# Performance work log

Measured on AMD Instinct MI355X. Metric: run time of the kernel, lower is better.

Reference implementation:

```python
import jax, jax.numpy as jnp
import numpy as np

N_GRAPHS = 64


def gcn_conv(x, W, b, src, dst, n_nodes):
    """PyG GCNConv: add self-loops, symmetric D^-1/2 (A+I) D^-1/2 normalization,
    linear transform, scatter-add aggregation at target nodes, plus bias."""
    xw = x @ W  # [N, out]  transform before propagate (PyG order)
    loop = jnp.arange(n_nodes, dtype=src.dtype)
    rows = jnp.concatenate([src, loop])  # message sources
    cols = jnp.concatenate([dst, loop])  # message targets
    deg = jax.ops.segment_sum(jnp.ones_like(cols, dtype=xw.dtype), cols,
                              num_segments=n_nodes)
    dinv = jnp.where(deg > 0, jax.lax.rsqrt(deg), 0.0)
    norm = dinv[rows] * dinv[cols]  # [E+N]
    msgs = norm[:, None] * xw[rows]  # gather + scale
    out = jax.ops.segment_sum(msgs, cols, num_segments=n_nodes)  # scatter-add
    return out + b


def global_mean_pool(x, batch, n_graphs):
    sums = jax.ops.segment_sum(x, batch, num_segments=n_graphs)
    cnts = jax.ops.segment_sum(jnp.ones((x.shape[0],), x.dtype), batch,
                               num_segments=n_graphs)
    return sums / jnp.maximum(cnts, 1.0)[:, None]


def setup_inputs() -> dict:
    key = jax.random.key(0)
    k1, k2, k3, k4, k5, k6 = jax.random.split(key, 6)
    N, E = 50000, 800000
    d_in, d_hid, d_out = 128, 128, 64
    x = jax.random.normal(k1, (N, d_in), dtype=jnp.float32)
    edge_index = jax.random.randint(k2, (2, E), 0, N, dtype=jnp.int64)
    batch = jnp.sort(jax.random.randint(k3, (N,), 0, N_GRAPHS, dtype=jnp.int64))
    # Glorot-ish init for GCN weights, zero bias (PyG default)
    W1 = jax.random.normal(k4, (d_in, d_hid), dtype=jnp.float32) / np.sqrt(d_in)
    b1 = jnp.zeros((d_hid,), jnp.float32)
    W2 = jax.random.normal(k5, (d_hid, d_out), dtype=jnp.float32) / np.sqrt(d_hid)
    b2 = jnp.zeros((d_out,), jnp.float32)
    return {"x": x, "edge_index": edge_index, "batch": batch,
            "W1": W1, "b1": b1, "W2": W2, "b2": b2}


def reference(x, edge_index, batch, W1, b1, W2, b2):
    n_nodes = x.shape[0]
    src, dst = edge_index[0], edge_index[1]
    h = jax.nn.relu(gcn_conv(x, W1, b1, src, dst, n_nodes))
    h = gcn_conv(h, W2, b2, src, dst, n_nodes)
    return global_mean_pool(h, batch, N_GRAPHS)
```

## Files before the change

### kernel.cpp

```cpp
#include <hip/hip_runtime.h>
#include <hip/hip_fp16.h>

typedef __attribute__((ext_vector_type(8))) short bf16x8;
typedef __attribute__((ext_vector_type(4))) float f32x4;

__device__ __forceinline__ unsigned short f2bf(float f) {
  unsigned u = __float_as_uint(f);
  u += 0x7FFFu + ((u >> 16) & 1u);
  return (unsigned short)(u >> 16);
}
__device__ __forceinline__ float bflo(unsigned u) { return __uint_as_float(u << 16); }
__device__ __forceinline__ float bfhi(unsigned u) { return __uint_as_float(u & 0xFFFF0000u); }
__device__ __forceinline__ float unpackw(unsigned pk) {
  return __half2float(__ushort_as_half((unsigned short)(pk >> 16)));
}

template <int CO, bool AF32>
__device__ __forceinline__ void gemm_body(const void* __restrict__ Aptr,
                                          const float* __restrict__ W,
                                          unsigned short* __restrict__ Y, int N,
                                          int bid, int tid, unsigned short* Wl) {
  constexpr int K = 128;
  constexpr int SP = K + 8;
  for (int i = tid; i < K * CO; i += 256) {
    int k = i / CO, n = i % CO;
    Wl[n * SP + k] = f2bf(W[i]);
  }
  __syncthreads();

  const int lane = tid & 63;
  const int quad = lane >> 4, l16 = lane & 15;
  const int mbase = bid * 64 + (tid >> 6) * 16;
  const int arow = min(mbase + l16, N - 1);

  bf16x8 afrag[4];
  if constexpr (AF32) {
    const float* A = (const float*)Aptr + (size_t)arow * K;
#pragma unroll
    for (int ks = 0; ks < 4; ks++) {
      const float4* p = (const float4*)(A + ks * 32 + quad * 8);
      float4 f0 = p[0], f1 = p[1];
      afrag[ks] = (bf16x8){(short)f2bf(f0.x), (short)f2bf(f0.y), (short)f2bf(f0.z), (short)f2bf(f0.w),
                           (short)f2bf(f1.x), (short)f2bf(f1.y), (short)f2bf(f1.z), (short)f2bf(f1.w)};
    }
  } else {
    const unsigned short* A = (const unsigned short*)Aptr + (size_t)arow * K;
#pragma unroll
    for (int ks = 0; ks < 4; ks++) afrag[ks] = *(const bf16x8*)(A + ks * 32 + quad * 8);
  }

#pragma unroll
  for (int ct = 0; ct < CO / 16; ct++) {
    f32x4 acc = {0.0f, 0.0f, 0.0f, 0.0f};
#pragma unroll
    for (int ks = 0; ks < 4; ks++) {
      bf16x8 b = *(const bf16x8*)(&Wl[(ct * 16 + l16) * SP + ks * 32 + quad * 8]);
      acc = __builtin_amdgcn_mfma_f32_16x16x32_bf16(afrag[ks], b, acc, 0, 0, 0);
    }
#pragma unroll
    for (int reg = 0; reg < 4; reg++) {
      int node = mbase + quad * 4 + reg;
      if (node < N) Y[(size_t)node * CO + ct * 16 + l16] = f2bf(acc[reg]);
    }
  }
}

__global__ __launch_bounds__(256) void k_mega1(const float* __restrict__ x,
                                               const float* __restrict__ W1,
                                               unsigned short* __restrict__ xw1b, int N,
                                               const int* __restrict__ src,
                                               const int* __restrict__ dst,
                                               int* __restrict__ cnt,
                                               unsigned short* __restrict__ colsrc, int E,
                                               const int* __restrict__ batch,
                                               int* __restrict__ firstIdx,
                                               int gM, int gE4) {
  __shared__ unsigned short Wl[128 * 136];
  const int bid = blockIdx.x, tid = threadIdx.x;
  if (bid < gM) {
    gemm_body<128, true>(x, W1, xw1b, N, bid, tid, Wl);
  } else if (bid < gM + gE4) {
    int e0 = (bid - gM) * 1024 + tid * 4;
    if (e0 + 3 < E) {
      int4 d4 = *(const int4*)(dst + e0);
      int4 s4 = *(const int4*)(src + e0);
      int r;
      r = atomicAdd(&cnt[d4.x], 1); if (r < 64) colsrc[(d4.x << 6) + r] = (unsigned short)s4.x;
      r = atomicAdd(&cnt[d4.y], 1); if (r < 64) colsrc[(d4.y << 6) + r] = (unsigned short)s4.y;
      r = atomicAdd(&cnt[d4.z], 1); if (r < 64) colsrc[(d4.z << 6) + r] = (unsigned short)s4.z;
      r = atomicAdd(&cnt[d4.w], 1); if (r < 64) colsrc[(d4.w << 6) + r] = (unsigned short)s4.w;
    } else {
      for (int e = e0; e < E; e++) {
        int d = dst[e];
        int r = atomicAdd(&cnt[d], 1);
        if (r < 64) colsrc[(d << 6) + r] = (unsigned short)src[e];
      }
    }
  } else {
    int n = (bid - gM - gE4) * 256 + tid;
    if (n < N) {
      int b = batch[n];
      if (n == 0 || batch[n - 1] != b) firstIdx[b] = n + 1;
    }
  }
}

__global__ __launch_bounds__(256) void k_agg128(const unsigned short* __restrict__ xwb,
                                                const int* __restrict__ cnt,
                                                const unsigned short* __restrict__ colsrc,
                                                const float* __restrict__ bias,
                                                unsigned short* __restrict__ out, int N) {
  const int tid = threadIdx.x;
  const int lane = tid & 63;
  const int gl = lane & 15;
  const int grp = lane >> 4;
  const int wv = tid >> 6;
  const int v = blockIdx.x * 16 + wv * 4 + grp;
  const int vc = min(v, N - 1);

  const int c = cnt[vc];
  const int jc = (v < N) ? min(c, 64) : 0;
  const float dv = rsqrtf((float)(c + 1));

  float acc[8];
  {
    const float d2 = dv * dv;
    uint4 s = *(const uint4*)((const char*)xwb + (((size_t)vc << 8) | (gl << 4)));
    acc[0] = d2 * bflo(s.x); acc[1] = d2 * bfhi(s.x);
    acc[2] = d2 * bflo(s.y); acc[3] = d2 * bfhi(s.y);
    acc[4] = d2 * bflo(s.z); acc[5] = d2 * bfhi(s.z);
    acc[6] = d2 * bflo(s.w); acc[7] = d2 * bfhi(s.w);
  }

  const int gbase = grp << 4;
  for (int base = 0; __any(base < jc); base += 16) {
    unsigned pk0 = 0u;
    if (base + gl < jc) {
      int s = colsrc[(vc << 6) + base + gl];
      float ws = rsqrtf((float)(cnt[s] + 1)) * dv;
      pk0 = (unsigned)s | ((unsigned)__half_as_ushort(__float2half_rn(ws)) << 16);
    }
    int mv = jc - base;
    mv = mv < 0 ? 0 : (mv > 16 ? 16 : mv);
    int mm = max(mv, __shfl_xor(mv, 16, 64));
    mm = max(mm, __shfl_xor(mm, 32, 64));
    const int rp = (mm + 7) & ~7;
    for (int t = 0; t < rp; t += 8) {
      uint4 rbuf[8];
      float wbuf[8];
#pragma unroll
      for (int r = 0; r < 8; r++) {
        unsigned pk = (unsigned)__shfl((int)pk0, gbase + t + r, 64);
        wbuf[r] = unpackw(pk);
        rbuf[r] = *(const uint4*)((const char*)xwb + (((pk & 0xFFFFu) << 8) | (gl << 4)));
      }
#pragma unroll
      for (int r = 0; r < 8; r++) {
        const float w = wbuf[r];
        const uint4 rr = rbuf[r];
        acc[0] += w * bflo(rr.x); acc[1] += w * bfhi(rr.x);
        acc[2] += w * bflo(rr.y); acc[3] += w * bfhi(rr.y);
        acc[4] += w * bflo(rr.z); acc[5] += w * bfhi(rr.z);
        acc[6] += w * bflo(rr.w); acc[7] += w * bfhi(rr.w);
      }
    }
  }

  if (v < N) {
    float4 b0 = ((const float4*)bias)[gl * 2];
    float4 b1 = ((const float4*)bias)[gl * 2 + 1];
    float a0 = fmaxf(acc[0] + b0.x, 0.f), a1 = fmaxf(acc[1] + b0.y, 0.f);
    float a2 = fmaxf(acc[2] + b0.z, 0.f), a3 = fmaxf(acc[3] + b0.w, 0.f);
    float a4 = fmaxf(acc[4] + b1.x, 0.f), a5 = fmaxf(acc[5] + b1.y, 0.f);
    float a6 = fmaxf(acc[6] + b1.z, 0.f), a7 = fmaxf(acc[7] + b1.w, 0.f);
    uint4 st;
    st.x = (unsigned)f2bf(a0) | ((unsigned)f2bf(a1) << 16);
    st.y = (unsigned)f2bf(a2) | ((unsigned)f2bf(a3) << 16);
    st.z = (unsigned)f2bf(a4) | ((unsigned)f2bf(a5) << 16);
    st.w = (unsigned)f2bf(a6) | ((unsigned)f2bf(a7) << 16);
    *(uint4*)((char*)out + (((size_t)v << 8) | (gl << 4))) = st;
  }
}

__global__ __launch_bounds__(256) void k_aggpool2(const unsigned short* __restrict__ h1b,
                                                  const int* __restrict__ cnt,
                                                  const unsigned short* __restrict__ colsrc,
                                                  const int* __restrict__ batch,
                                                  float* __restrict__ stage, int N) {
  __shared__ float sAcc[4][128];
  const int tid = threadIdx.x;
  const int lane = tid & 63;
  const int gl = lane & 15;
  const int grp = lane >> 4;
  const int wv = tid >> 6;
  const int v = blockIdx.x * 16 + wv * 4 + grp;
  const int vc = min(v, N - 1);

  const int c = cnt[vc];
  const int jc = (v < N) ? min(c, 64) : 0;
  const float dv = rsqrtf((float)(c + 1));

  float acc[8];
  {
    const float d2 = (v < N) ? dv * dv : 0.0f;
    uint4 s = *(const uint4*)((const char*)h1b + (((size_t)vc << 8) | (gl << 4)));
    acc[0] = d2 * bflo(s.x); acc[1] = d2 * bfhi(s.x);
    acc[2] = d2 * bflo(s.y); acc[3] = d2 * bfhi(s.y);
    acc[4] = d2 * bflo(s.z); acc[5] = d2 * bfhi(s.z);
    acc[6] = d2 * bflo(s.w); acc[7] = d2 * bfhi(s.w);
  }

  const int gbase = grp << 4;
  for (int base = 0; __any(base < jc); base += 16) {
    unsigned pk0 = 0u;
    if (base + gl < jc) {
      int s = colsrc[(vc << 6) + base + gl];
      float ws = rsqrtf((float)(cnt[s] + 1)) * dv;
      pk0 = (unsigned)s | ((unsigned)__half_as_ushort(__float2half_rn(ws)) << 16);
    }
    int mv = jc - base;
    mv = mv < 0 ? 0 : (mv > 16 ? 16 : mv);
    int mm = max(mv, __shfl_xor(mv, 16, 64));
    mm = max(mm, __shfl_xor(mm, 32, 64));
    const int rp = (mm + 7) & ~7;
    for (int t = 0; t < rp; t += 8) {
      uint4 rbuf[8];
      float wbuf[8];
#pragma unroll
      for (int r = 0; r < 8; r++) {
        unsigned pk = (unsigned)__shfl((int)pk0, gbase + t + r, 64);
        wbuf[r] = unpackw(pk);
        rbuf[r] = *(const uint4*)((const char*)h1b + (((pk & 0xFFFFu) << 8) | (gl << 4)));
      }
#pragma unroll
      for (int r = 0; r < 8; r++) {
        const float w = wbuf[r];
        const uint4 rr = rbuf[r];
        acc[0] += w * bflo(rr.x); acc[1] += w * bfhi(rr.x);
        acc[2] += w * bflo(rr.y); acc[3] += w * bfhi(rr.y);
        acc[4] += w * bflo(rr.z); acc[5] += w * bfhi(rr.z);
        acc[6] += w * bflo(rr.w); acc[7] += w * bfhi(rr.w);
      }
    }
  }

  const int v0 = blockIdx.x * 16;
  const bool uniform = (v0 + 15 < N) && (batch[v0] == batch[v0 + 15]);
  if (uniform) {
#pragma unroll
    for (int d = 16; d < 64; d <<= 1)
#pragma unroll
      for (int k = 0; k < 8; k++) acc[k] += __shfl_xor(acc[k], d, 64);
    if (grp == 0) {
#pragma unroll
      for (int k = 0; k < 8; k++) sAcc[wv][gl * 8 + k] = acc[k];
    }
    __syncthreads();
    if (wv == 0) {
      const int g = batch[v0];
      float t0 = sAcc[0][lane] + sAcc[1][lane] + sAcc[2][lane] + sAcc[3][lane];
      float t1 = sAcc[0][lane + 64] + sAcc[1][lane + 64] + sAcc[2][lane + 64] + sAcc[3][lane + 64];
      atomicAdd(&stage[g * 128 + lane], t0);
      atomicAdd(&stage[g * 128 + lane + 64], t1);
    }
  } else if (v < N) {
    const int b = batch[vc];
#pragma unroll
    for (int k = 0; k < 8; k++) atomicAdd(&stage[b * 128 + gl * 8 + k], acc[k]);
  }
}

__global__ void k_wout(const float* __restrict__ stage, const int* __restrict__ firstIdx,
                       const float* __restrict__ W2, const float* __restrict__ b2,
                       float* __restrict__ out, int N) {
  __shared__ float denom[64];
  __shared__ float red[256];
  const int tid = threadIdx.x;
  const int g = blockIdx.x;
  if (tid < 64) {
    int raw = firstIdx[tid];
    int fi = (raw > 0) ? raw - 1 : 0x7FFFFFFF;
    int m = fi;
#pragma unroll
    for (int d = 1; d < 64; d <<= 1) {
      int t = __shfl_down(m, d, 64);
      if (tid + d < 64) m = min(m, t);
    }
    int nxtm = __shfl_down(m, 1, 64);
    int nxt = (tid == 63) ? N : min(nxtm, N);
    int c = (fi == 0x7FFFFFFF) ? 0 : (nxt - fi);
    denom[tid] = fmaxf((float)c, 1.0f);
  }
  __syncthreads();
  const int j = tid & 63, kc = tid >> 6;
  float p = 0.0f;
#pragma unroll 8
  for (int k = kc * 32; k < kc * 32 + 32; k++)
    p += stage[g * 128 + k] * W2[k * 64 + j];
  red[tid] = p;
  __syncthreads();
  if (tid < 64) {
    float t = red[tid] + red[tid + 64] + red[tid + 128] + red[tid + 192];
    out[g * 64 + tid] = t / denom[g] + b2[tid];
  }
}


extern "C" void kernel_launch(void* const* d_in, const int* in_sizes, int n_in,
                              void* d_out, int out_size, void* d_ws, size_t ws_size,
                              hipStream_t stream) {
  const float* x     = (const float*)d_in[0];
  const int*   ei    = (const int*)d_in[1];
  const int*   batch = (const int*)d_in[2];
  const float* W1    = (const float*)d_in[3];
  const float* b1    = (const float*)d_in[4];
  const float* W2    = (const float*)d_in[5];
  const float* b2    = (const float*)d_in[6];

  const int N = in_sizes[2];
  const int E = in_sizes[1] / 2;
  const int* src  = ei;
  const int* dstv = ei + E;

  unsigned short* xw1b = (unsigned short*)d_ws;
  unsigned short* h1b  = xw1b + (size_t)N * 128;
  int*   cnt     = (int*)(h1b + (size_t)N * 128);
  int*   firstIdx= cnt + N;
  float* stage   = (float*)(firstIdx + 64);
  unsigned short* colsrc = (unsigned short*)(stage + 64 * 128);
  float* outp    = (float*)d_out;

  hipMemsetAsync(cnt, 0, (size_t)(N + 64 + 64 * 128) * sizeof(int), stream);

  const int gM  = (N + 63) / 64;
  const int gE4 = (E + 1023) / 1024;
  const int gN  = (N + 255) / 256;
  const int gA1 = (N + 15) / 16;

  k_mega1<<<gM + gE4 + gN, 256, 0, stream>>>(x, W1, xw1b, N, src, dstv, cnt,
                                             colsrc, E, batch, firstIdx, gM, gE4);

  k_agg128<<<gA1, 256, 0, stream>>>(xw1b, cnt, colsrc, b1, h1b, N);

  k_aggpool2<<<gA1, 256, 0, stream>>>(h1b, cnt, colsrc, batch, stage, N);

  k_wout<<<64, 256, 0, stream>>>(stage, firstIdx, W2, b2, outp, N);
}
```

Baseline: 190.2 us.

## Prefetch neighbor list once and double-buffer gather loads in aggregation kernels

Each lane now loads four neighbor indices at once with a ushort4 read and computes all their packed weights up front, replacing the per-16-neighbor chunk loop. The gather loop is double-buffered: the next batch of eight neighbor rows is loaded while FMAs run on the current batch, to hide gather latency. The cost is more live registers (two uint4[8] buffers), which may reduce occupancy.

```diff
diff --git a/kernel.cpp b/kernel.cpp
--- a/kernel.cpp
+++ b/kernel.cpp
@@ -105,6 +105,68 @@
   }
 }
 
+#define AGG_PREP(XWB_SHIFT)                                                         \
+  ushort4 s4v = *(const ushort4*)(colsrc + ((size_t)vc << 6) + gl * 4);             \
+  unsigned pk4[4];                                                                  \
+  {                                                                                 \
+    unsigned short se[4] = {s4v.x, s4v.y, s4v.z, s4v.w};                            \
+_Pragma("unroll")                                                                   \
+    for (int k = 0; k < 4; k++) {                                                   \
+      unsigned pk = 0u;                                                             \
+      int e = gl * 4 + k;                                                           \
+      if (e < jc) {                                                                 \
+        int s = se[k];                                                              \
+        float ws = rsqrtf((float)(cnt[s] + 1)) * dv;                                \
+        pk = (unsigned)s | ((unsigned)__half_as_ushort(__float2half_rn(ws)) << 16); \
+      }                                                                             \
+      pk4[k] = pk;                                                                  \
+    }                                                                               \
+  }                                                                                 \
+  int mm = jc;                                                                      \
+  mm = max(mm, __shfl_xor(mm, 16, 64));                                             \
+  mm = max(mm, __shfl_xor(mm, 32, 64));                                             \
+  const int nb = (mm + 7) >> 3;
+
+#define AGG_LOADB(bexp, R, WB, BASE, XWB_SHIFT)                                     \
+  {                                                                                 \
+    const int bb_ = (bexp);                                                         \
+_Pragma("unroll")                                                                   \
+    for (int r = 0; r < 8; r++) {                                                   \
+      unsigned pk = (unsigned)__shfl((int)pk4[r & 3], gbase + 2 * bb_ + (r >> 2), 64); \
+      WB[r] = unpackw(pk);                                                          \
+      R[r] = *(const uint4*)((const char*)(BASE) + (((pk & 0xFFFFu) << (XWB_SHIFT)) | (gl << 4))); \
+    }                                                                               \
+  }
+
+#define AGG_FMA(R, WB)                                                              \
+_Pragma("unroll")                                                                   \
+  for (int r = 0; r < 8; r++) {                                                     \
+    const float w = WB[r];                                                          \
+    const uint4 rr = R[r];                                                          \
+    acc[0] += w * bflo(rr.x); acc[1] += w * bfhi(rr.x);                             \
+    acc[2] += w * bflo(rr.y); acc[3] += w * bfhi(rr.y);                             \
+    acc[4] += w * bflo(rr.z); acc[5] += w * bfhi(rr.z);                             \
+    acc[6] += w * bflo(rr.w); acc[7] += w * bfhi(rr.w);                             \
+  }
+
+#define AGG_PIPELINE(BASE, XWB_SHIFT)                                               \
+  uint4 rA[8], rB[8];                                                               \
+  float wA[8], wB[8];                                                               \
+  if (nb > 0) {                                                                     \
+    AGG_LOADB(0, rA, wA, BASE, XWB_SHIFT);                                          \
+    int b = 0;                                                                      \
+    while (true) {                                                                  \
+      if (b + 1 < nb) AGG_LOADB(b + 1, rB, wB, BASE, XWB_SHIFT);                    \
+      AGG_FMA(rA, wA);                                                              \
+      b++;                                                                          \
+      if (b >= nb) break;                                                           \
+      if (b + 1 < nb) AGG_LOADB(b + 1, rA, wA, BASE, XWB_SHIFT);                    \
+      AGG_FMA(rB, wB);                                                              \
+      b++;                                                                          \
+      if (b >= nb) break;                                                           \
+    }                                                                               \
+  }
+
 __global__ __launch_bounds__(256) void k_agg128(const unsigned short* __restrict__ xwb,
                                                 const int* __restrict__ cnt,
                                                 const unsigned short* __restrict__ colsrc,
@@ -121,6 +183,7 @@
   const int c = cnt[vc];
   const int jc = (v < N) ? min(c, 64) : 0;
   const float dv = rsqrtf((float)(c + 1));
+  const int gbase = grp << 4;
 
   float acc[8];
   {
@@ -132,39 +195,8 @@
     acc[6] = d2 * bflo(s.w); acc[7] = d2 * bfhi(s.w);
   }
 
-  const int gbase = grp << 4;
-  for (int base = 0; __any(base < jc); base += 16) {
-    unsigned pk0 = 0u;
-    if (base + gl < jc) {
-      int s = colsrc[(vc << 6) + base + gl];
-      float ws = rsqrtf((float)(cnt[s] + 1)) * dv;
-      pk0 = (unsigned)s | ((unsigned)__half_as_ushort(__float2half_rn(ws)) << 16);
-    }
-    int mv = jc - base;
-    mv = mv < 0 ? 0 : (mv > 16 ? 16 : mv);
-    int mm = max(mv, __shfl_xor(mv, 16, 64));
-    mm = max(mm, __shfl_xor(mm, 32, 64));
-    const int rp = (mm + 7) & ~7;
-    for (int t = 0; t < rp; t += 8) {
-      uint4 rbuf[8];
-      float wbuf[8];
-#pragma unroll
-      for (int r = 0; r < 8; r++) {
-        unsigned pk = (unsigned)__shfl((int)pk0, gbase + t + r, 64);
-        wbuf[r] = unpackw(pk);
-        rbuf[r] = *(const uint4*)((const char*)xwb + (((pk & 0xFFFFu) << 8) | (gl << 4)));
-      }
-#pragma unroll
-      for (int r = 0; r < 8; r++) {
-        const float w = wbuf[r];
-        const uint4 rr = rbuf[r];
-        acc[0] += w * bflo(rr.x); acc[1] += w * bfhi(rr.x);
-        acc[2] += w * bflo(rr.y); acc[3] += w * bfhi(rr.y);
-        acc[4] += w * bflo(rr.z); acc[5] += w * bfhi(rr.z);
-        acc[6] += w * bflo(rr.w); acc[7] += w * bfhi(rr.w);
-      }
-    }
-  }
+  AGG_PREP(8)
+  AGG_PIPELINE(xwb, 8)
 
   if (v < N) {
     float4 b0 = ((const float4*)bias)[gl * 2];
@@ -199,6 +231,7 @@
   const int c = cnt[vc];
   const int jc = (v < N) ? min(c, 64) : 0;
   const float dv = rsqrtf((float)(c + 1));
+  const int gbase = grp << 4;
 
   float acc[8];
   {
@@ -210,39 +243,8 @@
     acc[6] = d2 * bflo(s.w); acc[7] = d2 * bfhi(s.w);
   }
 
-  const int gbase = grp << 4;
-  for (int base = 0; __any(base < jc); base += 16) {
-    unsigned pk0 = 0u;
-    if (base + gl < jc) {
-      int s = colsrc[(vc << 6) + base + gl];
-      float ws = rsqrtf((float)(cnt[s] + 1)) * dv;
-      pk0 = (unsigned)s | ((unsigned)__half_as_ushort(__float2half_rn(ws)) << 16);
-    }
-    int mv = jc - base;
-    mv = mv < 0 ? 0 : (mv > 16 ? 16 : mv);
-    int mm = max(mv, __shfl_xor(mv, 16, 64));
-    mm = max(mm, __shfl_xor(mm, 32, 64));
-    const int rp = (mm + 7) & ~7;
-    for (int t = 0; t < rp; t += 8) {
-      uint4 rbuf[8];
-      float wbuf[8];
-#pragma unroll
-      for (int r = 0; r < 8; r++) {
-        unsigned pk = (unsigned)__shfl((int)pk0, gbase + t + r, 64);
-        wbuf[r] = unpackw(pk);
-        rbuf[r] = *(const uint4*)((const char*)h1b + (((pk & 0xFFFFu) << 8) | (gl << 4)));
-      }
-#pragma unroll
-      for (int r = 0; r < 8; r++) {
-        const float w = wbuf[r];
-        const uint4 rr = rbuf[r];
-        acc[0] += w * bflo(rr.x); acc[1] += w * bfhi(rr.x);
-        acc[2] += w * bflo(rr.y); acc[3] += w * bfhi(rr.y);
-        acc[4] += w * bflo(rr.z); acc[5] += w * bfhi(rr.z);
-        acc[6] += w * bflo(rr.w); acc[7] += w * bfhi(rr.w);
-      }
-    }
-  }
+  AGG_PREP(8)
+  AGG_PIPELINE(h1b, 8)
 
   const int v0 = blockIdx.x * 16;
   const bool uniform = (v0 + 15 < N) && (batch[v0] == batch[v0 + 15]);
```

After: 202.1 us. 1.06x slower.

## Replace second-layer gather and pool with a graph-coefficient matrix and pooled GEMM

Applied to the files above, without the earlier changes.

The second GCN aggregation followed by mean pooling is rewritten algebraically. A per-node coefficient matrix Ct[N,64] is built by atomically adding each edge's normalisation weight (and the self-loop weight) into the column of the target node's graph. The pooled features then become Ct^T·h1, computed by a streaming partial-GEMM kernel with 256 blocks and reduced in k_wout. The Ct build is folded into the layer-1 aggregation launch, so the random 128-wide neighbour gathers of layer two are removed. In exchange it adds a 12.8 MB memset, 800k scattered float atomics, a larger workspace, and a GEMM with limited block parallelism.

```diff
diff --git a/kernel.cpp b/kernel.cpp
--- a/kernel.cpp
+++ b/kernel.cpp
@@ -11,6 +11,7 @@
 }
 __device__ __forceinline__ float bflo(unsigned u) { return __uint_as_float(u << 16); }
 __device__ __forceinline__ float bfhi(unsigned u) { return __uint_as_float(u & 0xFFFF0000u); }
+__device__ __forceinline__ float bf1(unsigned short h) { return __uint_as_float(((unsigned)h) << 16); }
 __device__ __forceinline__ float unpackw(unsigned pk) {
   return __half2float(__ushort_as_half((unsigned short)(pk >> 16)));
 }
@@ -105,175 +106,163 @@
   }
 }
 
-__global__ __launch_bounds__(256) void k_agg128(const unsigned short* __restrict__ xwb,
-                                                const int* __restrict__ cnt,
-                                                const unsigned short* __restrict__ colsrc,
-                                                const float* __restrict__ bias,
-                                                unsigned short* __restrict__ out, int N) {
-  const int tid = threadIdx.x;
-  const int lane = tid & 63;
-  const int gl = lane & 15;
-  const int grp = lane >> 4;
-  const int wv = tid >> 6;
-  const int v = blockIdx.x * 16 + wv * 4 + grp;
-  const int vc = min(v, N - 1);
-
-  const int c = cnt[vc];
-  const int jc = (v < N) ? min(c, 64) : 0;
-  const float dv = rsqrtf((float)(c + 1));
-
-  float acc[8];
-  {
-    const float d2 = dv * dv;
-    uint4 s = *(const uint4*)((const char*)xwb + (((size_t)vc << 8) | (gl << 4)));
-    acc[0] = d2 * bflo(s.x); acc[1] = d2 * bfhi(s.x);
-    acc[2] = d2 * bflo(s.y); acc[3] = d2 * bfhi(s.y);
-    acc[4] = d2 * bflo(s.z); acc[5] = d2 * bfhi(s.z);
-    acc[6] = d2 * bflo(s.w); acc[7] = d2 * bfhi(s.w);
-  }
-
-  const int gbase = grp << 4;
-  for (int base = 0; __any(base < jc); base += 16) {
-    unsigned pk0 = 0u;
-    if (base + gl < jc) {
-      int s = colsrc[(vc << 6) + base + gl];
-      float ws = rsqrtf((float)(cnt[s] + 1)) * dv;
-      pk0 = (unsigned)s | ((unsigned)__half_as_ushort(__float2half_rn(ws)) << 16);
-    }
-    int mv = jc - base;
-    mv = mv < 0 ? 0 : (mv > 16 ? 16 : mv);
-    int mm = max(mv, __shfl_xor(mv, 16, 64));
-    mm = max(mm, __shfl_xor(mm, 32, 64));
-    const int rp = (mm + 7) & ~7;
-    for (int t = 0; t < rp; t += 8) {
-      uint4 rbuf[8];
-      float wbuf[8];
-#pragma unroll
-      for (int r = 0; r < 8; r++) {
-        unsigned pk = (unsigned)__shfl((int)pk0, gbase + t + r, 64);
-        wbuf[r] = unpackw(pk);
-        rbuf[r] = *(const uint4*)((const char*)xwb + (((pk & 0xFFFFu) << 8) | (gl << 4)));
-      }
-#pragma unroll
-      for (int r = 0; r < 8; r++) {
-        const float w = wbuf[r];
-        const uint4 rr = rbuf[r];
-        acc[0] += w * bflo(rr.x); acc[1] += w * bfhi(rr.x);
-        acc[2] += w * bflo(rr.y); acc[3] += w * bfhi(rr.y);
-        acc[4] += w * bflo(rr.z); acc[5] += w * bfhi(rr.z);
-        acc[6] += w * bflo(rr.w); acc[7] += w * bfhi(rr.w);
-      }
-    }
-  }
-
-  if (v < N) {
-    float4 b0 = ((const float4*)bias)[gl * 2];
-    float4 b1 = ((const float4*)bias)[gl * 2 + 1];
-    float a0 = fmaxf(acc[0] + b0.x, 0.f), a1 = fmaxf(acc[1] + b0.y, 0.f);
-    float a2 = fmaxf(acc[2] + b0.z, 0.f), a3 = fmaxf(acc[3] + b0.w, 0.f);
-    float a4 = fmaxf(acc[4] + b1.x, 0.f), a5 = fmaxf(acc[5] + b1.y, 0.f);
-    float a6 = fmaxf(acc[6] + b1.z, 0.f), a7 = fmaxf(acc[7] + b1.w, 0.f);
-    uint4 st;
-    st.x = (unsigned)f2bf(a0) | ((unsigned)f2bf(a1) << 16);
-    st.y = (unsigned)f2bf(a2) | ((unsigned)f2bf(a3) << 16);
-    st.z = (unsigned)f2bf(a4) | ((unsigned)f2bf(a5) << 16);
-    st.w = (unsigned)f2bf(a6) | ((unsigned)f2bf(a7) << 16);
-    *(uint4*)((char*)out + (((size_t)v << 8) | (gl << 4))) = st;
-  }
-}
-
-__global__ __launch_bounds__(256) void k_aggpool2(const unsigned short* __restrict__ h1b,
-                                                  const int* __restrict__ cnt,
-                                                  const unsigned short* __restrict__ colsrc,
-                                                  const int* __restrict__ batch,
-                                                  float* __restrict__ stage, int N) {
-  __shared__ float sAcc[4][128];
-  const int tid = threadIdx.x;
-  const int lane = tid & 63;
-  const int gl = lane & 15;
-  const int grp = lane >> 4;
-  const int wv = tid >> 6;
-  const int v = blockIdx.x * 16 + wv * 4 + grp;
-  const int vc = min(v, N - 1);
-
-  const int c = cnt[vc];
-  const int jc = (v < N) ? min(c, 64) : 0;
-  const float dv = rsqrtf((float)(c + 1));
-
-  float acc[8];
-  {
-    const float d2 = (v < N) ? dv * dv : 0.0f;
-    uint4 s = *(const uint4*)((const char*)h1b + (((size_t)vc << 8) | (gl << 4)));
-    acc[0] = d2 * bflo(s.x); acc[1] = d2 * bfhi(s.x);
-    acc[2] = d2 * bflo(s.y); acc[3] = d2 * bfhi(s.y);
-    acc[4] = d2 * bflo(s.z); acc[5] = d2 * bfhi(s.z);
-    acc[6] = d2 * bflo(s.w); acc[7] = d2 * bfhi(s.w);
-  }
-
-  const int gbase = grp << 4;
-  for (int base = 0; __any(base < jc); base += 16) {
-    unsigned pk0 = 0u;
-    if (base + gl < jc) {
-      int s = colsrc[(vc << 6) + base + gl];
-      float ws = rsqrtf((float)(cnt[s] + 1)) * dv;
-      pk0 = (unsigned)s | ((unsigned)__half_as_ushort(__float2half_rn(ws)) << 16);
-    }
-    int mv = jc - base;
-    mv = mv < 0 ? 0 : (mv > 16 ? 16 : mv);
-    int mm = max(mv, __shfl_xor(mv, 16, 64));
-    mm = max(mm, __shfl_xor(mm, 32, 64));
-    const int rp = (mm + 7) & ~7;
-    for (int t = 0; t < rp; t += 8) {
-      uint4 rbuf[8];
-      float wbuf[8];
-#pragma unroll
-      for (int r = 0; r < 8; r++) {
-        unsigned pk = (unsigned)__shfl((int)pk0, gbase + t + r, 64);
-        wbuf[r] = unpackw(pk);
-        rbuf[r] = *(const uint4*)((const char*)h1b + (((pk & 0xFFFFu) << 8) | (gl << 4)));
-      }
-#pragma unroll
-      for (int r = 0; r < 8; r++) {
-        const float w = wbuf[r];
-        const uint4 rr = rbuf[r];
-        acc[0] += w * bflo(rr.x); acc[1] += w * bfhi(rr.x);
-        acc[2] += w * bflo(rr.y); acc[3] += w * bfhi(rr.y);
-        acc[4] += w * bflo(rr.z); acc[5] += w * bfhi(rr.z);
-        acc[6] += w * bflo(rr.w); acc[7] += w * bfhi(rr.w);
-      }
-    }
-  }
-
-  const int v0 = blockIdx.x * 16;
-  const bool uniform = (v0 + 15 < N) && (batch[v0] == batch[v0 + 15]);
-  if (uniform) {
-#pragma unroll
-    for (int d = 16; d < 64; d <<= 1)
-#pragma unroll
-      for (int k = 0; k < 8; k++) acc[k] += __shfl_xor(acc[k], d, 64);
-    if (grp == 0) {
-#pragma unroll
-      for (int k = 0; k < 8; k++) sAcc[wv][gl * 8 + k] = acc[k];
-    }
-    __syncthreads();
-    if (wv == 0) {
-      const int g = batch[v0];
-      float t0 = sAcc[0][lane] + sAcc[1][lane] + sAcc[2][lane] + sAcc[3][lane];
-      float t1 = sAcc[0][lane + 64] + sAcc[1][lane + 64] + sAcc[2][lane + 64] + sAcc[3][lane + 64];
-      atomicAdd(&stage[g * 128 + lane], t0);
-      atomicAdd(&stage[g * 128 + lane + 64], t1);
-    }
-  } else if (v < N) {
-    const int b = batch[vc];
-#pragma unroll
-    for (int k = 0; k < 8; k++) atomicAdd(&stage[b * 128 + gl * 8 + k], acc[k]);
-  }
-}
-
-__global__ void k_wout(const float* __restrict__ stage, const int* __restrict__ firstIdx,
+__global__ __launch_bounds__(256) void k_mega2(const unsigned short* __restrict__ xwb,
+                                               const int* __restrict__ cnt,
+                                               const unsigned short* __restrict__ colsrc,
+                                               const float* __restrict__ bias,
+                                               unsigned short* __restrict__ out, int N,
+                                               const int* __restrict__ src,
+                                               const int* __restrict__ dst,
+                                               const int* __restrict__ batch,
+                                               float* __restrict__ Ct, int E,
+                                               int gA, int gE4) {
+  const int bid = blockIdx.x, tid = threadIdx.x;
+  if (bid < gA) {
+    const int lane = tid & 63;
+    const int gl = lane & 15;
+    const int grp = lane >> 4;
+    const int wv = tid >> 6;
+    const int v = bid * 16 + wv * 4 + grp;
+    const int vc = min(v, N - 1);
+
+    const int c = cnt[vc];
+    const int jc = (v < N) ? min(c, 64) : 0;
+    const float dv = rsqrtf((float)(c + 1));
+
+    float acc[8];
+    {
+      const float d2 = dv * dv;
+      uint4 s = *(const uint4*)((const char*)xwb + (((size_t)vc << 8) | (gl << 4)));
+      acc[0] = d2 * bflo(s.x); acc[1] = d2 * bfhi(s.x);
+      acc[2] = d2 * bflo(s.y); acc[3] = d2 * bfhi(s.y);
+      acc[4] = d2 * bflo(s.z); acc[5] = d2 * bfhi(s.z);
+      acc[6] = d2 * bflo(s.w); acc[7] = d2 * bfhi(s.w);
+    }
+
+    const int gbase = grp << 4;
+    for (int base = 0; __any(base < jc); base += 16) {
+      unsigned pk0 = 0u;
+      if (base + gl < jc) {
+        int s = colsrc[(vc << 6) + base + gl];
+        float ws = rsqrtf((float)(cnt[s] + 1)) * dv;
+        pk0 = (unsigned)s | ((unsigned)__half_as_ushort(__float2half_rn(ws)) << 16);
+      }
+      int mv = jc - base;
+      mv = mv < 0 ? 0 : (mv > 16 ? 16 : mv);
+      int mm = max(mv, __shfl_xor(mv, 16, 64));
+      mm = max(mm, __shfl_xor(mm, 32, 64));
+      const int rp = (mm + 7) & ~7;
+      for (int t = 0; t < rp; t += 8) {
+        uint4 rbuf[8];
+        float wbuf[8];
+#pragma unroll
+        for (int r = 0; r < 8; r++) {
+          unsigned pk = (unsigned)__shfl((int)pk0, gbase + t + r, 64);
+          wbuf[r] = unpackw(pk);
+          rbuf[r] = *(const uint4*)((const char*)xwb + (((pk & 0xFFFFu) << 8) | (gl << 4)));
+        }
+#pragma unroll
+        for (int r = 0; r < 8; r++) {
+          const float w = wbuf[r];
+          const uint4 rr = rbuf[r];
+          acc[0] += w * bflo(rr.x); acc[1] += w * bfhi(rr.x);
+          acc[2] += w * bflo(rr.y); acc[3] += w * bfhi(rr.y);
+          acc[4] += w * bflo(rr.z); acc[5] += w * bfhi(rr.z);
+          acc[6] += w * bflo(rr.w); acc[7] += w * bfhi(rr.w);
+        }
+      }
+    }
+
+    if (v < N) {
+      float4 b0 = ((const float4*)bias)[gl * 2];
+      float4 b1 = ((const float4*)bias)[gl * 2 + 1];
+      float a0 = fmaxf(acc[0] + b0.x, 0.f), a1 = fmaxf(acc[1] + b0.y, 0.f);
+      float a2 = fmaxf(acc[2] + b0.z, 0.f), a3 = fmaxf(acc[3] + b0.w, 0.f);
+      float a4 = fmaxf(acc[4] + b1.x, 0.f), a5 = fmaxf(acc[5] + b1.y, 0.f);
+      float a6 = fmaxf(acc[6] + b1.z, 0.f), a7 = fmaxf(acc[7] + b1.w, 0.f);
+      uint4 st;
+      st.x = (unsigned)f2bf(a0) | ((unsigned)f2bf(a1) << 16);
+      st.y = (unsigned)f2bf(a2) | ((unsigned)f2bf(a3) << 16);
+      st.z = (unsigned)f2bf(a4) | ((unsigned)f2bf(a5) << 16);
+      st.w = (unsigned)f2bf(a6) | ((unsigned)f2bf(a7) << 16);
+      *(uint4*)((char*)out + (((size_t)v << 8) | (gl << 4))) = st;
+    }
+  } else if (bid < gA + gE4) {
+    int e0 = (bid - gA) * 1024 + tid * 4;
+    if (e0 + 3 < E) {
+      int4 s4 = *(const int4*)(src + e0);
+      int4 d4 = *(const int4*)(dst + e0);
+      {
+        float w = rsqrtf((float)(cnt[s4.x] + 1)) * rsqrtf((float)(cnt[d4.x] + 1));
+        atomicAdd(&Ct[(size_t)s4.x * 64 + batch[d4.x]], w);
+      }
+      {
+        float w = rsqrtf((float)(cnt[s4.y] + 1)) * rsqrtf((float)(cnt[d4.y] + 1));
+        atomicAdd(&Ct[(size_t)s4.y * 64 + batch[d4.y]], w);
+      }
+      {
+        float w = rsqrtf((float)(cnt[s4.z] + 1)) * rsqrtf((float)(cnt[d4.z] + 1));
+        atomicAdd(&Ct[(size_t)s4.z * 64 + batch[d4.z]], w);
+      }
+      {
+        float w = rsqrtf((float)(cnt[s4.w] + 1)) * rsqrtf((float)(cnt[d4.w] + 1));
+        atomicAdd(&Ct[(size_t)s4.w * 64 + batch[d4.w]], w);
+      }
+    } else {
+      for (int e = e0; e < E; e++) {
+        int s = src[e], d = dst[e];
+        float w = rsqrtf((float)(cnt[s] + 1)) * rsqrtf((float)(cnt[d] + 1));
+        atomicAdd(&Ct[(size_t)s * 64 + batch[d]], w);
+      }
+    }
+  } else {
+    int v = (bid - gA - gE4) * 256 + tid;
+    if (v < N) atomicAdd(&Ct[(size_t)v * 64 + batch[v]], 1.0f / (float)(cnt[v] + 1));
+  }
+}
+
+__global__ __launch_bounds__(256) void k_poolgemm(const unsigned short* __restrict__ h1b,
+                                                  const float* __restrict__ Ct,
+                                                  float* __restrict__ part, int N, int NB) {
+  const int bid = blockIdx.x, tid = threadIdx.x;
+  const int gq = tid & 15;
+  const int fs = tid >> 4;
+  const int chunk = (N + NB - 1) / NB;
+  const int k0 = bid * chunk;
+  const int k1 = min(k0 + chunk, N);
+
+  float acc[4][8];
+#pragma unroll
+  for (int gi = 0; gi < 4; gi++)
+#pragma unroll
+    for (int fi = 0; fi < 8; fi++) acc[gi][fi] = 0.0f;
+
+  for (int k = k0; k < k1; k++) {
+    float4 c4 = *(const float4*)(Ct + (size_t)k * 64 + gq * 4);
+    bf16x8 h8 = *(const bf16x8*)(h1b + (size_t)k * 128 + fs * 8);
+#pragma unroll
+    for (int fi = 0; fi < 8; fi++) {
+      float hv = bf1((unsigned short)h8[fi]);
+      acc[0][fi] += c4.x * hv;
+      acc[1][fi] += c4.y * hv;
+      acc[2][fi] += c4.z * hv;
+      acc[3][fi] += c4.w * hv;
+    }
+  }
+
+  float* pb = part + (size_t)bid * 8192;
+#pragma unroll
+  for (int gi = 0; gi < 4; gi++)
+#pragma unroll
+    for (int fi = 0; fi < 8; fi++)
+      pb[(gq * 4 + gi) * 128 + fs * 8 + fi] = acc[gi][fi];
+}
+
+__global__ void k_wout(const float* __restrict__ part, const int* __restrict__ firstIdx,
                        const float* __restrict__ W2, const float* __restrict__ b2,
-                       float* __restrict__ out, int N) {
+                       float* __restrict__ out, int N, int NB) {
   __shared__ float denom[64];
+  __shared__ float pooled[128];
   __shared__ float red[256];
   const int tid = threadIdx.x;
   const int g = blockIdx.x;
@@ -291,12 +280,21 @@
     int c = (fi == 0x7FFFFFFF) ? 0 : (nxt - fi);
     denom[tid] = fmaxf((float)c, 1.0f);
   }
+  if (tid < 128) {
+    float s0 = 0.f, s1 = 0.f;
+    for (int b = 0; b + 1 < NB; b += 2) {
+      s0 += part[(size_t)b * 8192 + g * 128 + tid];
+      s1 += part[(size_t)(b + 1) * 8192 + g * 128 + tid];
+    }
+    if (NB & 1) s0 += part[(size_t)(NB - 1) * 8192 + g * 128 + tid];
+    pooled[tid] = s0 + s1;
+  }
   __syncthreads();
   const int j = tid & 63, kc = tid >> 6;
   float p = 0.0f;
 #pragma unroll 8
   for (int k = kc * 32; k < kc * 32 + 32; k++)
-    p += stage[g * 128 + k] * W2[k * 64 + j];
+    p += pooled[k] * W2[k * 64 + j];
   red[tid] = p;
   __syncthreads();
   if (tid < 64) {
@@ -322,15 +320,18 @@
   const int* src  = ei;
   const int* dstv = ei + E;
 
+  const int NB = 256;
+
   unsigned short* xw1b = (unsigned short*)d_ws;
   unsigned short* h1b  = xw1b + (size_t)N * 128;
   int*   cnt     = (int*)(h1b + (size_t)N * 128);
   int*   firstIdx= cnt + N;
-  float* stage   = (float*)(firstIdx + 64);
-  unsigned short* colsrc = (unsigned short*)(stage + 64 * 128);
+  float* Ct      = (float*)(firstIdx + 64);
+  float* part    = Ct + (size_t)N * 64;
+  unsigned short* colsrc = (unsigned short*)(part + (size_t)NB * 8192);
   float* outp    = (float*)d_out;
 
-  hipMemsetAsync(cnt, 0, (size_t)(N + 64 + 64 * 128) * sizeof(int), stream);
+  hipMemsetAsync(cnt, 0, ((size_t)N + 64 + (size_t)N * 64) * sizeof(int), stream);
 
   const int gM  = (N + 63) / 64;
   const int gE4 = (E + 1023) / 1024;
@@ -340,9 +341,10 @@
   k_mega1<<<gM + gE4 + gN, 256, 0, stream>>>(x, W1, xw1b, N, src, dstv, cnt,
                                              colsrc, E, batch, firstIdx, gM, gE4);
 
-  k_agg128<<<gA1, 256, 0, stream>>>(xw1b, cnt, colsrc, b1, h1b, N);
-
-  k_aggpool2<<<gA1, 256, 0, stream>>>(h1b, cnt, colsrc, batch, stage, N);
-
-  k_wout<<<64, 256, 0, stream>>>(stage, firstIdx, W2, b2, outp, N);
-}
+  k_mega2<<<gA1 + gE4 + gN, 256, 0, stream>>>(xw1b, cnt, colsrc, b1, h1b, N,
+                                              src, dstv, batch, Ct, E, gA1, gE4);
+
+  k_poolgemm<<<NB, 256, 0, stream>>>(h1b, Ct, part, N, NB);
+
+  k_wout<<<64, 256, 0, stream>>>(part, firstIdx, W2, b2, outp, N, NB);
+}
```

Result: slower. 310.6 us (+63.3%).
